# Kernel optimization log

Measured on AMD Instinct MI355X. Metric: run time of the kernel, lower is better.

The kernel has to match this reference:

```python
import jax, jax.numpy as jnp
import numpy as np
import math

S = 64.0
M = 0.5
COS_M = math.cos(M)
SIN_M = math.sin(M)
TH = math.cos(math.pi - M)
MM = math.sin(math.pi - M) * M
BATCH = 512
EMBED = 512
NUM_CLASSES = 100000

def setup_inputs() -> dict:
    key = jax.random.key(0)
    k1, k2, k3 = jax.random.split(key, 3)
    inp = jax.random.normal(k1, (BATCH, EMBED), dtype=jnp.float32)
    label = jax.random.randint(k2, (BATCH,), 0, NUM_CLASSES, dtype=jnp.int64)
    # xavier_uniform_ on [num_classes, embedding_size]
    limit = math.sqrt(6.0 / (NUM_CLASSES + EMBED))
    weight = jax.random.uniform(k3, (NUM_CLASSES, EMBED), dtype=jnp.float32,
                                minval=-limit, maxval=limit)
    return {"input": inp, "label": label, "weight": weight}


def reference(input, label, weight):
    # F.normalize(weight) along dim=1 (eps=1e-12), then F.linear
    w_norm = weight / jnp.maximum(jnp.linalg.norm(weight, axis=1, keepdims=True), 1e-12)
    cosine = input @ w_norm.T  # [B, C]
    sine = jnp.sqrt(jnp.clip(1.0 - cosine * cosine, 0.0, 1.0))
    phi = cosine * COS_M - sine * SIN_M
    phi = jnp.where(cosine > TH, phi, cosine - MM)
    one_hot = jax.nn.one_hot(label, NUM_CLASSES, dtype=cosine.dtype)  # [B, C]
    output = (one_hot * phi + (1.0 - one_hot) * cosine) * S
    logp = jax.nn.log_softmax(output, axis=-1)
    # NLLLoss with mean reduction
    loss = -jnp.mean(jnp.take_along_axis(logp, label[:, None], axis=1)[:, 0])
    return (output, loss)
```

## Files before the change

### kernel.cpp

```cpp
#include <hip/hip_runtime.h>

#define NCLS   100000
#define CPAD   100096
#define EMB    512
#define BATCH  512
#define NBN    782
#define NJ     1564

#define S_F     64.0f
#define COS_M_F 0.8775825619f
#define SIN_M_F 0.4794255386f
#define TH_F   (-0.8775825619f)
#define MM_F    0.2397127693f

#define WS_ABF   0ull
#define WS_INV   524288ull
#define WS_PMAX  924672ull
#define WS_PSUM  4127744ull
#define WS_NLL   7330816ull
#define WS_EXACT 7332864ull
#define WS_WBF   7334912ull
#define WS_NEED_FAST 109833216ull
typedef unsigned short ushort_t;

typedef __attribute__((ext_vector_type(8))) short bf16x8;
typedef __attribute__((ext_vector_type(4))) float floatx4;

__device__ __forceinline__ unsigned short f2bf(float f) {
    union { float f; unsigned int u; } c; c.f = f;
    unsigned int r = c.u + 0x7FFFu + ((c.u >> 16) & 1u);
    return (unsigned short)(r >> 16);
}

__device__ __forceinline__ void load_lds16(const void* g, void* l) {
    __builtin_amdgcn_global_load_lds(
        (const __attribute__((address_space(1))) void*)g,
        (__attribute__((address_space(3))) void*)l, 16, 0, 0);
}

__global__ __launch_bounds__(256) void cvt_input_kernel(
    const float* __restrict__ in, ushort_t* __restrict__ Abf) {
    int gid = blockIdx.x * 256 + threadIdx.x;
    float4 f = ((const float4*)in)[gid];
    uint2 u;
    u.x = (unsigned)f2bf(f.x) | ((unsigned)f2bf(f.y) << 16);
    u.y = (unsigned)f2bf(f.z) | ((unsigned)f2bf(f.w) << 16);
    ((uint2*)Abf)[gid] = u;
}

template <bool WRITE_WBF>
__global__ __launch_bounds__(256) void norms_kernel(
    const float* __restrict__ W, ushort_t* __restrict__ Wbf,
    float* __restrict__ inv_norm) {
    int t = threadIdx.x;
    int lane = t & 63;
    int r = blockIdx.x * 4 + (t >> 6);
    float4 f0 = make_float4(0.f, 0.f, 0.f, 0.f);
    float4 f1 = make_float4(0.f, 0.f, 0.f, 0.f);
    float ssq = 0.f;
    if (r < NCLS) {
        const float4* rp = (const float4*)(W + (size_t)r * EMB);
        f0 = rp[lane * 2];
        f1 = rp[lane * 2 + 1];
        ssq = f0.x*f0.x + f0.y*f0.y + f0.z*f0.z + f0.w*f0.w
            + f1.x*f1.x + f1.y*f1.y + f1.z*f1.z + f1.w*f1.w;
    }
    #pragma unroll
    for (int msk = 1; msk < 64; msk <<= 1) ssq += __shfl_xor(ssq, msk);
    float inv = 0.f;
    if (r < NCLS) inv = 1.0f / fmaxf(sqrtf(ssq), 1e-12f);
    if (lane == 0 && r < CPAD) inv_norm[r] = inv;
    if (WRITE_WBF) {
        uint4 u;
        u.x = (unsigned)f2bf(f0.x*inv) | ((unsigned)f2bf(f0.y*inv) << 16);
        u.y = (unsigned)f2bf(f0.z*inv) | ((unsigned)f2bf(f0.w*inv) << 16);
        u.z = (unsigned)f2bf(f1.x*inv) | ((unsigned)f2bf(f1.y*inv) << 16);
        u.w = (unsigned)f2bf(f1.z*inv) | ((unsigned)f2bf(f1.w*inv) << 16);
        ((uint4*)(Wbf + (size_t)r * EMB))[lane] = u;
    }
}

__global__ __launch_bounds__(256) void exact_label_kernel(
    const float* __restrict__ input, const float* __restrict__ W,
    const float* __restrict__ inv_norm, const int* __restrict__ label,
    float* __restrict__ exact_val) {
    const int t = threadIdx.x;
    const int lane = t & 63;
    const int row = blockIdx.x * 4 + (t >> 6);
    const int lab = label[row];
    const float4* ip = (const float4*)(input + (size_t)row * EMB);
    const float4* wp = (const float4*)(W + (size_t)lab * EMB);
    float4 a0 = ip[lane], a1 = ip[64 + lane];
    float4 b0 = wp[lane], b1 = wp[64 + lane];
    float dot = a0.x*b0.x + a0.y*b0.y + a0.z*b0.z + a0.w*b0.w
              + a1.x*b1.x + a1.y*b1.y + a1.z*b1.z + a1.w*b1.w;
    #pragma unroll
    for (int msk = 1; msk < 64; msk <<= 1) dot += __shfl_xor(dot, msk);
    if (lane == 0) {
        float c = dot * inv_norm[lab];
        float sine = sqrtf(fmaxf(1.0f - c * c, 0.0f));
        float phi = c * COS_M_F - sine * SIN_M_F;
        phi = (c > TH_F) ? phi : (c - MM_F);
        exact_val[row] = S_F * phi;
    }
}

template <int BSRC>
__global__ __launch_bounds__(256) void gemm_kernel(
    const ushort_t* __restrict__ Abf,
    const float*    __restrict__ Wfp,
    const ushort_t* __restrict__ Wbf,
    const float*    __restrict__ inv_norm,
    const int*      __restrict__ label,
    const float*    __restrict__ exact_val,
    float*          __restrict__ out,
    float* __restrict__ pmax, float* __restrict__ psum) {
    __shared__ ushort_t As[128][64];
    __shared__ ushort_t Bs[128][64];

    const int t = threadIdx.x;
    const int lane = t & 63, wid = t >> 6;
    const int wr = wid >> 1, wc = wid & 1;
    const int bid = blockIdx.x;
    const int mblk = bid & 3, nblk = bid >> 2;
    const int m0 = mblk * 128;
    const int c0 = nblk * 128;

    floatx4 acc[4][4] = {};

    for (int k0 = 0; k0 < EMB; k0 += 64) {
        __syncthreads();
        #pragma unroll
        for (int r = 0; r < 4; ++r) {
            int i = r * 256 + t;
            int row = i >> 3, col = (i & 7) << 3;
            const ushort_t* gp = Abf + (size_t)(m0 + row) * EMB + k0 + col;
            load_lds16(gp, (char*)(&As[0][0]) + (size_t)(r * 256 + wid * 64) * 16);
        }
        if constexpr (BSRC == 0) {
            #pragma unroll
            for (int r = 0; r < 4; ++r) {
                int i = r * 256 + t;
                int row = i >> 3, col = (i & 7) << 3;
                const ushort_t* gp = Wbf + (size_t)(c0 + row) * EMB + k0 + col;
                load_lds16(gp, (char*)(&Bs[0][0]) + (size_t)(r * 256 + wid * 64) * 16);
            }
        } else {
            #pragma unroll
            for (int r = 0; r < 4; ++r) {
                int i = r * 256 + t;
                int row = i >> 3, ck = (i & 7) << 3;
                int c = c0 + row;
                bf16x8 v = {0, 0, 0, 0, 0, 0, 0, 0};
                if (c < NCLS) {
                    const float* gp = Wfp + (size_t)c * EMB + k0 + ck;
                    float4 a = ((const float4*)gp)[0];
                    float4 b = ((const float4*)gp)[1];
                    v[0] = (short)f2bf(a.x); v[1] = (short)f2bf(a.y);
                    v[2] = (short)f2bf(a.z); v[3] = (short)f2bf(a.w);
                    v[4] = (short)f2bf(b.x); v[5] = (short)f2bf(b.y);
                    v[6] = (short)f2bf(b.z); v[7] = (short)f2bf(b.w);
                }
                *(bf16x8*)(&Bs[row][ck]) = v;
            }
        }
        __syncthreads();
        #pragma unroll
        for (int kk = 0; kk < 2; ++kk) {
            const int ko = kk * 32 + ((lane >> 4) << 3);
            bf16x8 af[4], bw[4];
            #pragma unroll
            for (int m = 0; m < 4; ++m)
                af[m] = *(const bf16x8*)(&As[wr * 64 + m * 16 + (lane & 15)][ko]);
            #pragma unroll
            for (int n = 0; n < 4; ++n)
                bw[n] = *(const bf16x8*)(&Bs[wc * 64 + n * 16 + (lane & 15)][ko]);
            #pragma unroll
            for (int m = 0; m < 4; ++m)
                #pragma unroll
                for (int n = 0; n < 4; ++n)
                    acc[m][n] = __builtin_amdgcn_mfma_f32_16x16x32_bf16(
                        af[m], bw[n], acc[m][n], 0, 0, 0);
        }
    }

    const int q = lane >> 4, fr = lane & 15;
    const int jcol = (nblk << 1) | wc;
    #pragma unroll
    for (int m = 0; m < 4; ++m) {
        #pragma unroll
        for (int j = 0; j < 4; ++j) {
            const int grow = m0 + wr * 64 + m * 16 + q * 4 + j;
            const int lab = label[grow];
            const float exv = exact_val[grow];
            float o[4]; int cc[4];
            float vmax = -1e30f;
            #pragma unroll
            for (int n = 0; n < 4; ++n) {
                const int col = c0 + wc * 64 + n * 16 + fr;
                float cosv = acc[m][n][j];
                if (BSRC == 1) cosv *= inv_norm[col];
                float val = (col == lab) ? exv : (S_F * cosv);
                o[n] = val; cc[n] = col;
                if (col < NCLS) {
                    out[(size_t)grow * NCLS + col] = val;
                    vmax = fmaxf(vmax, val);
                }
            }
            #pragma unroll
            for (int msk = 1; msk < 16; msk <<= 1)
                vmax = fmaxf(vmax, __shfl_xor(vmax, msk));
            float vsum = 0.0f;
            #pragma unroll
            for (int n = 0; n < 4; ++n)
                if (cc[n] < NCLS) vsum += __expf(o[n] - vmax);
            #pragma unroll
            for (int msk = 1; msk < 16; msk <<= 1)
                vsum += __shfl_xor(vsum, msk);
            if (fr == 0) {
                pmax[(size_t)grow * NJ + jcol] = vmax;
                psum[(size_t)grow * NJ + jcol] = vsum;
            }
        }
    }
}

__global__ __launch_bounds__(256) void row_lse_kernel(
    const float* __restrict__ pmax, const float* __restrict__ psum,
    const float* __restrict__ out, const int* __restrict__ label,
    float* __restrict__ nll) {
    const int row = blockIdx.x;
    const int t = threadIdx.x;
    float m = -1e30f, s = 0.f;
    for (int j = t; j < NJ; j += 256) {
        float pm = pmax[(size_t)row * NJ + j];
        float ps = psum[(size_t)row * NJ + j];
        float nm = fmaxf(m, pm);
        s = s * __expf(m - nm) + ps * __expf(pm - nm);
        m = nm;
    }
    #pragma unroll
    for (int msk = 1; msk < 64; msk <<= 1) {
        float om = __shfl_xor(m, msk), os = __shfl_xor(s, msk);
        float nm = fmaxf(m, om);
        s = s * __expf(m - nm) + os * __expf(om - nm);
        m = nm;
    }
    __shared__ float sm[4], ss[4];
    const int lane = t & 63, wid = t >> 6;
    if (lane == 0) { sm[wid] = m; ss[wid] = s; }
    __syncthreads();
    if (t == 0) {
        float M = sm[0], SS = ss[0];
        #pragma unroll
        for (int w = 1; w < 4; ++w) {
            float nm = fmaxf(M, sm[w]);
            SS = SS * __expf(M - nm) + ss[w] * __expf(sm[w] - nm);
            M = nm;
        }
        float lse = M + logf(SS);
        float tgt = out[(size_t)row * NCLS + label[row]];
        nll[row] = lse - tgt;
    }
}

__global__ __launch_bounds__(512) void loss_kernel(
    const float* __restrict__ nll, float* __restrict__ out_loss) {
    const int t = threadIdx.x;
    float v = nll[t];
    #pragma unroll
    for (int msk = 1; msk < 64; msk <<= 1) v += __shfl_xor(v, msk);
    __shared__ float sv[8];
    if ((t & 63) == 0) sv[t >> 6] = v;
    __syncthreads();
    if (t == 0) {
        float s = 0.f;
        #pragma unroll
        for (int w = 0; w < 8; ++w) s += sv[w];
        out_loss[0] = s / 512.0f;
    }
}

extern "C" void kernel_launch(void* const* d_in, const int* in_sizes, int n_in,
                              void* d_out, int out_size, void* d_ws, size_t ws_size,
                              hipStream_t stream) {
    const float* input  = (const float*)d_in[0];
    const int*   label  = (const int*)d_in[1];
    const float* weight = (const float*)d_in[2];
    float* out = (float*)d_out;
    char* ws = (char*)d_ws;
    ushort_t* Abf     = (ushort_t*)(ws + WS_ABF);
    float*    invn    = (float*)(ws + WS_INV);
    float*    pmax    = (float*)(ws + WS_PMAX);
    float*    psum    = (float*)(ws + WS_PSUM);
    float*    nll     = (float*)(ws + WS_NLL);
    float*    exv     = (float*)(ws + WS_EXACT);
    ushort_t* Wbf     = (ushort_t*)(ws + WS_WBF);
    const bool fast = ws_size >= WS_NEED_FAST;

    cvt_input_kernel<<<dim3(256), dim3(256), 0, stream>>>(input, Abf);
    if (fast) {
        norms_kernel<true><<<dim3(CPAD / 4), dim3(256), 0, stream>>>(weight, Wbf, invn);
        exact_label_kernel<<<dim3(128), dim3(256), 0, stream>>>(input, weight, invn, label, exv);
        gemm_kernel<0><<<dim3(4 * NBN), dim3(256), 0, stream>>>(
            Abf, weight, Wbf, invn, label, exv, out, pmax, psum);
    } else {
        norms_kernel<false><<<dim3(CPAD / 4), dim3(256), 0, stream>>>(weight, Wbf, invn);
        exact_label_kernel<<<dim3(128), dim3(256), 0, stream>>>(input, weight, invn, label, exv);
        gemm_kernel<1><<<dim3(4 * NBN), dim3(256), 0, stream>>>(
            Abf, weight, Wbf, invn, label, exv, out, pmax, psum);
    }
    row_lse_kernel<<<dim3(512), dim3(256), 0, stream>>>(pmax, psum, out, label, nll);
    loss_kernel<<<dim3(1), dim3(512), 0, stream>>>(nll, out + (out_size - 1));
}
```

Before: 513.8 us.

## Chunk weight normalization with GEMM, swizzle LDS and XCD, nontemporal output stores

```diff
diff --git a/kernel.cpp b/kernel.cpp
--- a/kernel.cpp
+++ b/kernel.cpp
@@ -14,15 +14,14 @@
 #define MM_F    0.2397127693f
 
 #define WS_ABF   0ull
-#define WS_INV   524288ull
-#define WS_PMAX  924672ull
-#define WS_PSUM  4127744ull
-#define WS_NLL   7330816ull
-#define WS_EXACT 7332864ull
+#define WS_PMAX  524288ull
+#define WS_PSUM  3727360ull
+#define WS_NLL   6930432ull
+#define WS_EXACT 6932480ull
+#define WS_INV   6934528ull
 #define WS_WBF   7334912ull
-#define WS_NEED_FAST 109833216ull
+
 typedef unsigned short ushort_t;
-
 typedef __attribute__((ext_vector_type(8))) short bf16x8;
 typedef __attribute__((ext_vector_type(4))) float floatx4;
 
@@ -36,6 +35,13 @@
     __builtin_amdgcn_global_load_lds(
         (const __attribute__((address_space(1))) void*)g,
         (__attribute__((address_space(3))) void*)l, 16, 0, 0);
+}
+
+__device__ __forceinline__ int xcd_swizzle(int b0, int nwg) {
+    const int q = nwg >> 3, r = nwg & 7;
+    const int x = b0 & 7, o = b0 >> 3;
+    const int base = (x < r) ? x * (q + 1) : r * (q + 1) + (x - r) * q;
+    return base + o;
 }
 
 __global__ __launch_bounds__(256) void cvt_input_kernel(
@@ -48,42 +54,9 @@
     ((uint2*)Abf)[gid] = u;
 }
 
-template <bool WRITE_WBF>
-__global__ __launch_bounds__(256) void norms_kernel(
-    const float* __restrict__ W, ushort_t* __restrict__ Wbf,
-    float* __restrict__ inv_norm) {
-    int t = threadIdx.x;
-    int lane = t & 63;
-    int r = blockIdx.x * 4 + (t >> 6);
-    float4 f0 = make_float4(0.f, 0.f, 0.f, 0.f);
-    float4 f1 = make_float4(0.f, 0.f, 0.f, 0.f);
-    float ssq = 0.f;
-    if (r < NCLS) {
-        const float4* rp = (const float4*)(W + (size_t)r * EMB);
-        f0 = rp[lane * 2];
-        f1 = rp[lane * 2 + 1];
-        ssq = f0.x*f0.x + f0.y*f0.y + f0.z*f0.z + f0.w*f0.w
-            + f1.x*f1.x + f1.y*f1.y + f1.z*f1.z + f1.w*f1.w;
-    }
-    #pragma unroll
-    for (int msk = 1; msk < 64; msk <<= 1) ssq += __shfl_xor(ssq, msk);
-    float inv = 0.f;
-    if (r < NCLS) inv = 1.0f / fmaxf(sqrtf(ssq), 1e-12f);
-    if (lane == 0 && r < CPAD) inv_norm[r] = inv;
-    if (WRITE_WBF) {
-        uint4 u;
-        u.x = (unsigned)f2bf(f0.x*inv) | ((unsigned)f2bf(f0.y*inv) << 16);
-        u.y = (unsigned)f2bf(f0.z*inv) | ((unsigned)f2bf(f0.w*inv) << 16);
-        u.z = (unsigned)f2bf(f1.x*inv) | ((unsigned)f2bf(f1.y*inv) << 16);
-        u.w = (unsigned)f2bf(f1.z*inv) | ((unsigned)f2bf(f1.w*inv) << 16);
-        ((uint4*)(Wbf + (size_t)r * EMB))[lane] = u;
-    }
-}
-
 __global__ __launch_bounds__(256) void exact_label_kernel(
     const float* __restrict__ input, const float* __restrict__ W,
-    const float* __restrict__ inv_norm, const int* __restrict__ label,
-    float* __restrict__ exact_val) {
+    const int* __restrict__ label, float* __restrict__ exact_val) {
     const int t = threadIdx.x;
     const int lane = t & 63;
     const int row = blockIdx.x * 4 + (t >> 6);
@@ -94,10 +67,15 @@
     float4 b0 = wp[lane], b1 = wp[64 + lane];
     float dot = a0.x*b0.x + a0.y*b0.y + a0.z*b0.z + a0.w*b0.w
               + a1.x*b1.x + a1.y*b1.y + a1.z*b1.z + a1.w*b1.w;
-    #pragma unroll
-    for (int msk = 1; msk < 64; msk <<= 1) dot += __shfl_xor(dot, msk);
+    float ssq = b0.x*b0.x + b0.y*b0.y + b0.z*b0.z + b0.w*b0.w
+              + b1.x*b1.x + b1.y*b1.y + b1.z*b1.z + b1.w*b1.w;
+    #pragma unroll
+    for (int msk = 1; msk < 64; msk <<= 1) {
+        dot += __shfl_xor(dot, msk);
+        ssq += __shfl_xor(ssq, msk);
+    }
     if (lane == 0) {
-        float c = dot * inv_norm[lab];
+        float c = dot / fmaxf(sqrtf(ssq), 1e-12f);
         float sine = sqrtf(fmaxf(1.0f - c * c, 0.0f));
         float phi = c * COS_M_F - sine * SIN_M_F;
         phi = (c > TH_F) ? phi : (c - MM_F);
@@ -105,25 +83,71 @@
     }
 }
 
+__global__ __launch_bounds__(256) void norms_chunk_kernel(
+    const float* __restrict__ W, ushort_t* __restrict__ Wbfc, int cls0) {
+    const int t = threadIdx.x, lane = t & 63;
+    const int rl = blockIdx.x * 4 + (t >> 6);
+    const int r = cls0 + rl;
+    float4 f0 = make_float4(0.f, 0.f, 0.f, 0.f);
+    float4 f1 = make_float4(0.f, 0.f, 0.f, 0.f);
+    float ssq = 0.f;
+    if (r < NCLS) {
+        const float4* rp = (const float4*)(W + (size_t)r * EMB);
+        f0 = rp[lane * 2];
+        f1 = rp[lane * 2 + 1];
+        ssq = f0.x*f0.x + f0.y*f0.y + f0.z*f0.z + f0.w*f0.w
+            + f1.x*f1.x + f1.y*f1.y + f1.z*f1.z + f1.w*f1.w;
+    }
+    #pragma unroll
+    for (int msk = 1; msk < 64; msk <<= 1) ssq += __shfl_xor(ssq, msk);
+    float inv = 0.f;
+    if (r < NCLS) inv = 1.0f / fmaxf(sqrtf(ssq), 1e-12f);
+    uint4 u;
+    u.x = (unsigned)f2bf(f0.x*inv) | ((unsigned)f2bf(f0.y*inv) << 16);
+    u.y = (unsigned)f2bf(f0.z*inv) | ((unsigned)f2bf(f0.w*inv) << 16);
+    u.z = (unsigned)f2bf(f1.x*inv) | ((unsigned)f2bf(f1.y*inv) << 16);
+    u.w = (unsigned)f2bf(f1.z*inv) | ((unsigned)f2bf(f1.w*inv) << 16);
+    ((uint4*)(Wbfc + (size_t)rl * EMB))[lane] = u;
+}
+
+__global__ __launch_bounds__(256) void norms_inv_kernel(
+    const float* __restrict__ W, float* __restrict__ inv_norm) {
+    const int t = threadIdx.x, lane = t & 63;
+    const int r = blockIdx.x * 4 + (t >> 6);
+    float ssq = 0.f;
+    if (r < NCLS) {
+        const float4* rp = (const float4*)(W + (size_t)r * EMB);
+        float4 f0 = rp[lane * 2], f1 = rp[lane * 2 + 1];
+        ssq = f0.x*f0.x + f0.y*f0.y + f0.z*f0.z + f0.w*f0.w
+            + f1.x*f1.x + f1.y*f1.y + f1.z*f1.z + f1.w*f1.w;
+    }
+    #pragma unroll
+    for (int msk = 1; msk < 64; msk <<= 1) ssq += __shfl_xor(ssq, msk);
+    if (lane == 0 && r < CPAD)
+        inv_norm[r] = (r < NCLS) ? 1.0f / fmaxf(sqrtf(ssq), 1e-12f) : 0.f;
+}
+
 template <int BSRC>
 __global__ __launch_bounds__(256) void gemm_kernel(
     const ushort_t* __restrict__ Abf,
     const float*    __restrict__ Wfp,
-    const ushort_t* __restrict__ Wbf,
+    const ushort_t* __restrict__ Wbfc,
     const float*    __restrict__ inv_norm,
     const int*      __restrict__ label,
     const float*    __restrict__ exact_val,
     float*          __restrict__ out,
-    float* __restrict__ pmax, float* __restrict__ psum) {
-    __shared__ ushort_t As[128][64];
-    __shared__ ushort_t Bs[128][64];
+    float* __restrict__ pmax, float* __restrict__ psum,
+    int nblk0) {
+    __shared__ ushort_t As[128 * 64];
+    __shared__ ushort_t Bs[128 * 64];
 
     const int t = threadIdx.x;
     const int lane = t & 63, wid = t >> 6;
     const int wr = wid >> 1, wc = wid & 1;
-    const int bid = blockIdx.x;
-    const int mblk = bid & 3, nblk = bid >> 2;
+    const int wg = xcd_swizzle(blockIdx.x, gridDim.x);
+    const int mblk = wg & 3, nblkL = wg >> 2;
     const int m0 = mblk * 128;
+    const int nblk = nblk0 + nblkL;
     const int c0 = nblk * 128;
 
     floatx4 acc[4][4] = {};
@@ -132,28 +156,31 @@
         __syncthreads();
         #pragma unroll
         for (int r = 0; r < 4; ++r) {
-            int i = r * 256 + t;
-            int row = i >> 3, col = (i & 7) << 3;
-            const ushort_t* gp = Abf + (size_t)(m0 + row) * EMB + k0 + col;
-            load_lds16(gp, (char*)(&As[0][0]) + (size_t)(r * 256 + wid * 64) * 16);
+            const int i = r * 256 + t;
+            const int row = i >> 3;
+            const int ls = (i & 7) ^ (row & 7);
+            const ushort_t* gp = Abf + (size_t)(m0 + row) * EMB + k0 + (ls << 3);
+            load_lds16(gp, (char*)As + (size_t)(r * 256 + wid * 64) * 16);
         }
         if constexpr (BSRC == 0) {
             #pragma unroll
             for (int r = 0; r < 4; ++r) {
-                int i = r * 256 + t;
-                int row = i >> 3, col = (i & 7) << 3;
-                const ushort_t* gp = Wbf + (size_t)(c0 + row) * EMB + k0 + col;
-                load_lds16(gp, (char*)(&Bs[0][0]) + (size_t)(r * 256 + wid * 64) * 16);
+                const int i = r * 256 + t;
+                const int row = i >> 3;
+                const int ls = (i & 7) ^ (row & 7);
+                const ushort_t* gp = Wbfc + (size_t)(nblkL * 128 + row) * EMB + k0 + (ls << 3);
+                load_lds16(gp, (char*)Bs + (size_t)(r * 256 + wid * 64) * 16);
             }
         } else {
             #pragma unroll
             for (int r = 0; r < 4; ++r) {
-                int i = r * 256 + t;
-                int row = i >> 3, ck = (i & 7) << 3;
-                int c = c0 + row;
+                const int i = r * 256 + t;
+                const int row = i >> 3;
+                const int ls = i & 7;
+                const int c = c0 + row;
                 bf16x8 v = {0, 0, 0, 0, 0, 0, 0, 0};
                 if (c < NCLS) {
-                    const float* gp = Wfp + (size_t)c * EMB + k0 + ck;
+                    const float* gp = Wfp + (size_t)c * EMB + k0 + (ls << 3);
                     float4 a = ((const float4*)gp)[0];
                     float4 b = ((const float4*)gp)[1];
                     v[0] = (short)f2bf(a.x); v[1] = (short)f2bf(a.y);
@@ -161,20 +188,25 @@
                     v[4] = (short)f2bf(b.x); v[5] = (short)f2bf(b.y);
                     v[6] = (short)f2bf(b.z); v[7] = (short)f2bf(b.w);
                 }
-                *(bf16x8*)(&Bs[row][ck]) = v;
+                *(bf16x8*)((char*)Bs + (size_t)row * 128 + ((ls ^ (row & 7)) << 4)) = v;
             }
         }
         __syncthreads();
+        const int fr = lane & 15, q = lane >> 4, sx = fr & 7;
         #pragma unroll
         for (int kk = 0; kk < 2; ++kk) {
-            const int ko = kk * 32 + ((lane >> 4) << 3);
+            const int lslot = kk * 4 + q;
             bf16x8 af[4], bw[4];
             #pragma unroll
-            for (int m = 0; m < 4; ++m)
-                af[m] = *(const bf16x8*)(&As[wr * 64 + m * 16 + (lane & 15)][ko]);
-            #pragma unroll
-            for (int n = 0; n < 4; ++n)
-                bw[n] = *(const bf16x8*)(&Bs[wc * 64 + n * 16 + (lane & 15)][ko]);
+            for (int m = 0; m < 4; ++m) {
+                const int row = wr * 64 + m * 16 + fr;
+                af[m] = *(const bf16x8*)((const char*)As + (size_t)row * 128 + ((lslot ^ sx) << 4));
+            }
+            #pragma unroll
+            for (int n = 0; n < 4; ++n) {
+                const int row = wc * 64 + n * 16 + fr;
+                bw[n] = *(const bf16x8*)((const char*)Bs + (size_t)row * 128 + ((lslot ^ sx) << 4));
+            }
             #pragma unroll
             for (int m = 0; m < 4; ++m)
                 #pragma unroll
@@ -184,7 +216,7 @@
         }
     }
 
-    const int q = lane >> 4, fr = lane & 15;
+    const int fr = lane & 15, q = lane >> 4;
     const int jcol = (nblk << 1) | wc;
     #pragma unroll
     for (int m = 0; m < 4; ++m) {
@@ -203,7 +235,7 @@
                 float val = (col == lab) ? exv : (S_F * cosv);
                 o[n] = val; cc[n] = col;
                 if (col < NCLS) {
-                    out[(size_t)grow * NCLS + col] = val;
+                    __builtin_nontemporal_store(val, &out[(size_t)grow * NCLS + col]);
                     vmax = fmaxf(vmax, val);
                 }
             }
@@ -289,26 +321,39 @@
     const float* weight = (const float*)d_in[2];
     float* out = (float*)d_out;
     char* ws = (char*)d_ws;
-    ushort_t* Abf     = (ushort_t*)(ws + WS_ABF);
-    float*    invn    = (float*)(ws + WS_INV);
-    float*    pmax    = (float*)(ws + WS_PMAX);
-    float*    psum    = (float*)(ws + WS_PSUM);
-    float*    nll     = (float*)(ws + WS_NLL);
-    float*    exv     = (float*)(ws + WS_EXACT);
-    ushort_t* Wbf     = (ushort_t*)(ws + WS_WBF);
-    const bool fast = ws_size >= WS_NEED_FAST;
+    ushort_t* Abf  = (ushort_t*)(ws + WS_ABF);
+    float*    pmax = (float*)(ws + WS_PMAX);
+    float*    psum = (float*)(ws + WS_PSUM);
+    float*    nll  = (float*)(ws + WS_NLL);
+    float*    exv  = (float*)(ws + WS_EXACT);
+    float*    invn = (float*)(ws + WS_INV);
+    ushort_t* Wbf  = (ushort_t*)(ws + WS_WBF);
+
+    size_t avail = ws_size > WS_WBF ? ws_size - WS_WBF : 0;
+    int nch = 0, per = 0;
+    const int cand[5] = {1, 2, 4, 8, 16};
+    for (int ci = 0; ci < 5; ++ci) {
+        int p = (NBN + cand[ci] - 1) / cand[ci];
+        if ((size_t)p * 128 * EMB * 2 <= avail) { nch = cand[ci]; per = p; break; }
+    }
 
     cvt_input_kernel<<<dim3(256), dim3(256), 0, stream>>>(input, Abf);
-    if (fast) {
-        norms_kernel<true><<<dim3(CPAD / 4), dim3(256), 0, stream>>>(weight, Wbf, invn);
-        exact_label_kernel<<<dim3(128), dim3(256), 0, stream>>>(input, weight, invn, label, exv);
-        gemm_kernel<0><<<dim3(4 * NBN), dim3(256), 0, stream>>>(
-            Abf, weight, Wbf, invn, label, exv, out, pmax, psum);
+    exact_label_kernel<<<dim3(128), dim3(256), 0, stream>>>(input, weight, label, exv);
+
+    if (nch) {
+        for (int c = 0; c < nch; ++c) {
+            const int nb0 = c * per;
+            int pc = NBN - nb0; if (pc > per) pc = per;
+            if (pc <= 0) break;
+            norms_chunk_kernel<<<dim3(pc * 32), dim3(256), 0, stream>>>(
+                weight, Wbf, nb0 * 128);
+            gemm_kernel<0><<<dim3(4 * pc), dim3(256), 0, stream>>>(
+                Abf, weight, Wbf, invn, label, exv, out, pmax, psum, nb0);
+        }
     } else {
-        norms_kernel<false><<<dim3(CPAD / 4), dim3(256), 0, stream>>>(weight, Wbf, invn);
-        exact_label_kernel<<<dim3(128), dim3(256), 0, stream>>>(input, weight, invn, label, exv);
+        norms_inv_kernel<<<dim3(CPAD / 4), dim3(256), 0, stream>>>(weight, invn);
         gemm_kernel<1><<<dim3(4 * NBN), dim3(256), 0, stream>>>(
-            Abf, weight, Wbf, invn, label, exv, out, pmax, psum);
+            Abf, weight, Wbf, invn, label, exv, out, pmax, psum, 0);
     }
     row_lse_kernel<<<dim3(512), dim3(256), 0, stream>>>(pmax, psum, out, label, nll);
     loss_kernel<<<dim3(1), dim3(512), 0, stream>>>(nll, out + (out_size - 1));
```

After: 510.6 us. Within noise of the previous version (-0.6%).
